# Kernel optimization log

Measured on AMD Instinct MI355X. Metric: run time of the kernel, lower is better.

Reference implementation:

```python
import jax, jax.numpy as jnp
import numpy as np

NEG_SLOPE = 0.2


def gat_conv(x, src, dst, W, a_src, a_dst, b, num_nodes):
    # x: [N, Fin], W: [Fin, Fout], a_src/a_dst: [Fout], b: [Fout]
    h = x @ W                                   # [N, Fout]
    alpha_s = h @ a_src                         # [N]
    alpha_d = h @ a_dst                         # [N]
    e = alpha_s[src] + alpha_d[dst]             # [E]
    e = jnp.where(e > 0, e, NEG_SLOPE * e)      # LeakyReLU(0.2)
    # segment softmax over edges grouped by destination node
    m = jax.ops.segment_max(e, dst, num_segments=num_nodes)   # [N]
    e = jnp.exp(e - m[dst])
    s = jax.ops.segment_sum(e, dst, num_segments=num_nodes)   # [N]
    alpha = e / s[dst]                          # [E] (every node has a self-loop)
    out = jax.ops.segment_sum(h[src] * alpha[:, None], dst, num_segments=num_nodes)
    return out + b


def setup_inputs() -> dict:
    key = jax.random.key(0)
    ks = jax.random.split(key, 10)
    N, E = 50000, 640000
    Fin, Fh, Fout = 128, 128, 64
    x = jax.random.normal(ks[0], (N, Fin), dtype=jnp.float32)
    edge_index = jax.random.randint(ks[1], (2, E), 0, N, dtype=jnp.int64)
    g = 1.0 / np.sqrt(Fin)
    W1 = jax.random.normal(ks[2], (Fin, Fh), dtype=jnp.float32) * g
    a1_src = jax.random.normal(ks[3], (Fh,), dtype=jnp.float32) * 0.1
    a1_dst = jax.random.normal(ks[4], (Fh,), dtype=jnp.float32) * 0.1
    b1 = jnp.zeros((Fh,), dtype=jnp.float32)
    g2 = 1.0 / np.sqrt(Fh)
    W2 = jax.random.normal(ks[5], (Fh, Fout), dtype=jnp.float32) * g2
    a2_src = jax.random.normal(ks[6], (Fout,), dtype=jnp.float32) * 0.1
    a2_dst = jax.random.normal(ks[7], (Fout,), dtype=jnp.float32) * 0.1
    b2 = jnp.zeros((Fout,), dtype=jnp.float32)
    return {"x": x, "edge_index": edge_index, "W1": W1, "a1_src": a1_src,
            "a1_dst": a1_dst, "b1": b1, "W2": W2, "a2_src": a2_src,
            "a2_dst": a2_dst, "b2": b2}


def reference(x, edge_index, W1, a1_src, a1_dst, b1, W2, a2_src, a2_dst, b2):
    N = x.shape[0]
    loops = jnp.arange(N, dtype=edge_index.dtype)
    src = jnp.concatenate([edge_index[0], loops])  # add self-loops (PyG default)
    dst = jnp.concatenate([edge_index[1], loops])
    h = gat_conv(x, src, dst, W1, a1_src, a1_dst, b1, N)
    h = jax.nn.relu(h)
    # F.dropout(0.1) skipped: deterministic (eval-mode) reference
    out = gat_conv(h, src, dst, W2, a2_src, a2_dst, b2, N)
    return out
```

## Files before the change

kernel.cpp:

```cpp
#include <hip/hip_runtime.h>

#define LEAK 0.2f

static __device__ __forceinline__ float leaky(float e) { return e > 0.f ? e : LEAK * e; }

static __device__ __forceinline__ unsigned f2bf(float f) {
    union { float f; unsigned u; } v; v.f = f;
    return (v.u + 0x7FFFu + ((v.u >> 16) & 1u)) >> 16;
}
static __device__ __forceinline__ float bflo(unsigned u) {
    union { unsigned x; float f; } v; v.x = u << 16; return v.f;
}
static __device__ __forceinline__ float bfhi(unsigned u) {
    union { unsigned x; float f; } v; v.x = u & 0xFFFF0000u; return v.f;
}

using bf16x8 = __attribute__((ext_vector_type(8))) short;
using f32x4 = __attribute__((ext_vector_type(4))) float;

__global__ __launch_bounds__(256) void k_prep(int* __restrict__ counts, int n,
                                              const int* __restrict__ ei, int nwords_check,
                                              int* __restrict__ flag,
                                              const float* __restrict__ W1,
                                              unsigned short* __restrict__ Wt1,
                                              const float* __restrict__ W2,
                                              unsigned short* __restrict__ Wt2, int NB) {
    int bid = blockIdx.x;
    int t = threadIdx.x;
    if (bid == 0) {
        if (t < 64) {
            int bad = 0;
            for (int i = 1 + 2 * t; i < nwords_check; i += 128) bad |= (ei[i] != 0);
            unsigned long long anybad = __ballot(bad != 0);
            if (t == 0) *flag = (anybad == 0ULL) ? 1 : 0;
        }
        return;
    }
    if (bid <= NB) {
        int i = (bid - 1) * 256 + t;
        if (i < n) counts[i] = 0;
        return;
    }
    if (bid <= NB + 4) {
        int q = bid - (NB + 1);
        int c = t & 127, ksub = t >> 7;
        int k0 = q * 32 + ksub * 16;
        union { unsigned short s[16]; uint4 v[2]; } u;
#pragma unroll
        for (int j = 0; j < 16; ++j) u.s[j] = (unsigned short)f2bf(W1[(size_t)(k0 + j) * 128 + c]);
        uint4* dst = (uint4*)(Wt1 + (size_t)c * 128 + k0);
        dst[0] = u.v[0];
        dst[1] = u.v[1];
        return;
    }
    {
        int q = bid - (NB + 5);
        int c = t & 63, ksub = t >> 6;
        int k0 = q * 64 + ksub * 16;
        union { unsigned short s[16]; uint4 v[2]; } u;
#pragma unroll
        for (int j = 0; j < 16; ++j) u.s[j] = (unsigned short)f2bf(W2[(size_t)(k0 + j) * 64 + c]);
        uint4* dst = (uint4*)(Wt2 + (size_t)c * 128 + k0);
        dst[0] = u.v[0];
        dst[1] = u.v[1];
        return;
    }
}

__global__ void k_count(const int* __restrict__ ei, const int* __restrict__ flag,
                        int* __restrict__ counts, int E) {
    int e = blockIdx.x * 256 + threadIdx.x;
    if (e >= E) return;
    int is64 = *flag;
    int d = is64 ? ei[(size_t)2 * E + 2 * e] : ei[(size_t)E + e];
    atomicAdd(&counts[d], 1);
}

__global__ void k_scan1(const int* __restrict__ counts, int* __restrict__ incl,
                        int* __restrict__ bsums, int n) {
    __shared__ int s[256];
    int t = threadIdx.x;
    int g = blockIdx.x * 256 + t;
    int v = (g < n) ? counts[g] : 0;
    s[t] = v;
    __syncthreads();
    for (int off = 1; off < 256; off <<= 1) {
        int add = (t >= off) ? s[t - off] : 0;
        __syncthreads();
        s[t] += add;
        __syncthreads();
    }
    if (g < n) incl[g] = s[t];
    if (t == 255) bsums[blockIdx.x] = s[255];
}

__global__ void k_scan2(int* __restrict__ bsums, int nb) {
    __shared__ int s[256];
    int t = threadIdx.x;
    int v = (t < nb) ? bsums[t] : 0;
    s[t] = v;
    __syncthreads();
    for (int off = 1; off < 256; off <<= 1) {
        int add = (t >= off) ? s[t - off] : 0;
        __syncthreads();
        s[t] += add;
        __syncthreads();
    }
    int excl = (t == 0) ? 0 : s[t - 1];
    if (t < nb) bsums[t] = excl;
}

__global__ void k_scan3(const int* __restrict__ incl, const int* __restrict__ bsums,
                        const int* __restrict__ counts, int* __restrict__ rowptr,
                        int* __restrict__ fillpos, int n) {
    int g = blockIdx.x * 256 + threadIdx.x;
    if (g < n) {
        int inc = incl[g] + bsums[blockIdx.x];
        rowptr[g + 1] = inc;
        fillpos[g] = inc - counts[g];
    }
    if (g == 0) rowptr[0] = 0;
}

__global__ void k_fill(const int* __restrict__ ei, const int* __restrict__ flag,
                       int* __restrict__ fillpos, int* __restrict__ colv, int E) {
    int e = blockIdx.x * 256 + threadIdx.x;
    if (e >= E) return;
    int is64 = *flag;
    int s = is64 ? ei[2 * e] : ei[e];
    int d = is64 ? ei[(size_t)2 * E + 2 * e] : ei[(size_t)E + e];
    int p = atomicAdd(&fillpos[d], 1);
    colv[p] = s;
}

template <int F, bool AF32>
__global__ __launch_bounds__(256) void k_gemm_mfma(const void* __restrict__ Xv,
                                                   const unsigned short* __restrict__ Wt,
                                                   const float* __restrict__ asrc,
                                                   const float* __restrict__ adst,
                                                   unsigned short* __restrict__ Hb,
                                                   float* __restrict__ out_s,
                                                   float* __restrict__ out_d, int n) {
    constexpr int K = 128;
    constexpr int KP = K + 8;
    constexpr int NT = F / 16;
    __shared__ unsigned short wsT[F * KP];
    int t = threadIdx.x;
    int w = t >> 6, lane = t & 63;
    int lrow = lane & 15, kg = lane >> 4;
    long long row0 = (long long)blockIdx.x * 64;

#pragma unroll
    for (int i = t; i < F * (K / 8); i += 256) {
        int c = i / (K / 8), j8 = i % (K / 8);
        uint4 v = ((const uint4*)(Wt + (size_t)c * K))[j8];
        *(uint4*)&wsT[c * KP + 8 * j8] = v;
    }
    __syncthreads();

    long long grow = row0 + w * 16 + lrow;
    bool rowok = grow < n;

    f32x4 acc[NT];
#pragma unroll
    for (int i = 0; i < NT; ++i) acc[i] = (f32x4){0.f, 0.f, 0.f, 0.f};

#pragma unroll
    for (int ks = 0; ks < K / 32; ++ks) {
        bf16x8 af;
        if constexpr (AF32) {
            const float* Xp = (const float*)Xv + grow * K + ks * 32 + kg * 8;
            float4 x0 = make_float4(0.f, 0.f, 0.f, 0.f), x1 = x0;
            if (rowok) {
                x0 = ((const float4*)Xp)[0];
                x1 = ((const float4*)Xp)[1];
            }
            af = (bf16x8){(short)f2bf(x0.x), (short)f2bf(x0.y), (short)f2bf(x0.z), (short)f2bf(x0.w),
                          (short)f2bf(x1.x), (short)f2bf(x1.y), (short)f2bf(x1.z), (short)f2bf(x1.w)};
        } else {
            uint4 u = make_uint4(0, 0, 0, 0);
            if (rowok) {
                const unsigned short* Xp = (const unsigned short*)Xv + grow * K + ks * 32 + kg * 8;
                u = *(const uint4*)Xp;
            }
            af = *(bf16x8*)&u;
        }
#pragma unroll
        for (int nt = 0; nt < NT; ++nt) {
            const unsigned short* bp = &wsT[(nt * 16 + lrow) * KP + ks * 32 + kg * 8];
            uint4 ub = *(const uint4*)bp;
            bf16x8 bf = *(bf16x8*)&ub;
            acc[nt] = __builtin_amdgcn_mfma_f32_16x16x32_bf16(af, bf, acc[nt], 0, 0, 0);
        }
    }

    {
        float ps[4] = {0.f, 0.f, 0.f, 0.f}, pd[4] = {0.f, 0.f, 0.f, 0.f};
#pragma unroll
        for (int nt = 0; nt < NT; ++nt) {
            float asv = asrc[nt * 16 + lrow];
            float adv = adst[nt * 16 + lrow];
#pragma unroll
            for (int i = 0; i < 4; ++i) {
                ps[i] = fmaf(acc[nt][i], asv, ps[i]);
                pd[i] = fmaf(acc[nt][i], adv, pd[i]);
            }
        }
#pragma unroll
        for (int off = 1; off < 16; off <<= 1) {
#pragma unroll
            for (int i = 0; i < 4; ++i) {
                ps[i] += __shfl_xor(ps[i], off);
                pd[i] += __shfl_xor(pd[i], off);
            }
        }
        if (lrow == 0) {
#pragma unroll
            for (int i = 0; i < 4; ++i) {
                long long r = row0 + w * 16 + kg * 4 + i;
                if (r < n) {
                    out_s[r] = ps[i];
                    out_d[r] = pd[i];
                }
            }
        }
    }

    int r0 = w * 16 + kg * 4;
#pragma unroll
    for (int nt = 0; nt < NT; ++nt) {
        int c = nt * 16 + lrow;
#pragma unroll
        for (int i = 0; i < 4; ++i) {
            long long r = row0 + r0 + i;
            if (r < n) Hb[r * F + c] = (unsigned short)f2bf(acc[nt][i]);
        }
    }
}

template <int F, bool RELU, bool OB>
__global__ __launch_bounds__(256) void k_agg(const int* __restrict__ rowptr,
                                             const int* __restrict__ colv,
                                             const float* __restrict__ as_,
                                             const float* __restrict__ ad_,
                                             const unsigned* __restrict__ Hu,
                                             const float* __restrict__ bias,
                                             void* __restrict__ OUT, int n) {
    constexpr int FG8 = F / 8;
    constexpr int GRP = 64 / FG8;
    int node = blockIdx.x * 4 + (threadIdx.x >> 6);
    int lane = threadIdx.x & 63;
    if (node >= n) return;
    int rs = rowptr[node], re = rowptr[node + 1];
    int deg = re - rs;
    float adi = ad_[node];
    float e_self = leaky(as_[node] + adi);

    int scol = node;
    float e_l = -3.0e38f;
    if (lane < deg) {
        scol = colv[rs + lane];
        e_l = leaky(as_[scol] + adi);
    }
    float m = fmaxf(e_l, e_self);
    for (int base = 64; base < deg; base += 64) {
        if (base + lane < deg) m = fmaxf(m, leaky(as_[colv[rs + base + lane]] + adi));
    }
#pragma unroll
    for (int off = 32; off; off >>= 1) m = fmaxf(m, __shfl_xor(m, off));

    float p_l = (lane < deg) ? __expf(e_l - m) : 0.f;
    float ssum = p_l;
    for (int base = 64; base < deg; base += 64) {
        if (base + lane < deg) ssum += __expf(leaky(as_[colv[rs + base + lane]] + adi) - m);
    }
#pragma unroll
    for (int off = 32; off; off >>= 1) ssum += __shfl_xor(ssum, off);
    float pself = __expf(e_self - m);
    ssum += pself;
    float inv = 1.f / ssum;
    float w_l = p_l * inv;
    float wself = pself * inv;

    int grp = lane / FG8;
    int fg = lane % FG8;
    const uint4* __restrict__ H16 = (const uint4*)Hu;
    float a0, a1, a2, a3, a4, a5, a6, a7;
    {
        uint4 hv = H16[(size_t)node * FG8 + fg];
        float ws0 = (grp == 0) ? wself : 0.f;
        a0 = ws0 * bflo(hv.x); a1 = ws0 * bfhi(hv.x);
        a2 = ws0 * bflo(hv.y); a3 = ws0 * bfhi(hv.y);
        a4 = ws0 * bflo(hv.z); a5 = ws0 * bfhi(hv.z);
        a6 = ws0 * bflo(hv.w); a7 = ws0 * bfhi(hv.w);
    }

    int cnt = deg < 64 ? deg : 64;
    constexpr int STEP = 4 * GRP;
    int cntr = (cnt + STEP - 1) / STEP * STEP;
#pragma unroll 1
    for (int i = 0; i < cntr; i += STEP) {
        int i0 = i + grp, i1 = i + GRP + grp, i2 = i + 2 * GRP + grp, i3 = i + 3 * GRP + grp;
        int s0 = __shfl(scol, i0), s1 = __shfl(scol, i1);
        int s2 = __shfl(scol, i2), s3 = __shfl(scol, i3);
        float w0 = __shfl(w_l, i0), w1 = __shfl(w_l, i1);
        float w2 = __shfl(w_l, i2), w3 = __shfl(w_l, i3);
        uint4 g0 = H16[(size_t)s0 * FG8 + fg];
        uint4 g1 = H16[(size_t)s1 * FG8 + fg];
        uint4 g2 = H16[(size_t)s2 * FG8 + fg];
        uint4 g3 = H16[(size_t)s3 * FG8 + fg];
        a0 = fmaf(w0, bflo(g0.x), a0); a1 = fmaf(w0, bfhi(g0.x), a1);
        a2 = fmaf(w0, bflo(g0.y), a2); a3 = fmaf(w0, bfhi(g0.y), a3);
        a4 = fmaf(w0, bflo(g0.z), a4); a5 = fmaf(w0, bfhi(g0.z), a5);
        a6 = fmaf(w0, bflo(g0.w), a6); a7 = fmaf(w0, bfhi(g0.w), a7);
        a0 = fmaf(w1, bflo(g1.x), a0); a1 = fmaf(w1, bfhi(g1.x), a1);
        a2 = fmaf(w1, bflo(g1.y), a2); a3 = fmaf(w1, bfhi(g1.y), a3);
        a4 = fmaf(w1, bflo(g1.z), a4); a5 = fmaf(w1, bfhi(g1.z), a5);
        a6 = fmaf(w1, bflo(g1.w), a6); a7 = fmaf(w1, bfhi(g1.w), a7);
        a0 = fmaf(w2, bflo(g2.x), a0); a1 = fmaf(w2, bfhi(g2.x), a1);
        a2 = fmaf(w2, bflo(g2.y), a2); a3 = fmaf(w2, bfhi(g2.y), a3);
        a4 = fmaf(w2, bflo(g2.z), a4); a5 = fmaf(w2, bfhi(g2.z), a5);
        a6 = fmaf(w2, bflo(g2.w), a6); a7 = fmaf(w2, bfhi(g2.w), a7);
        a0 = fmaf(w3, bflo(g3.x), a0); a1 = fmaf(w3, bfhi(g3.x), a1);
        a2 = fmaf(w3, bflo(g3.y), a2); a3 = fmaf(w3, bfhi(g3.y), a3);
        a4 = fmaf(w3, bflo(g3.z), a4); a5 = fmaf(w3, bfhi(g3.z), a5);
        a6 = fmaf(w3, bflo(g3.w), a6); a7 = fmaf(w3, bfhi(g3.w), a7);
    }
    for (int j = rs + 64; j < re; ++j) {
        int s = colv[j];
        float w = __expf(leaky(as_[s] + adi) - m) * inv;
        float we = (grp == 0) ? w : 0.f;
        uint4 g = H16[(size_t)s * FG8 + fg];
        a0 = fmaf(we, bflo(g.x), a0); a1 = fmaf(we, bfhi(g.x), a1);
        a2 = fmaf(we, bflo(g.y), a2); a3 = fmaf(we, bfhi(g.y), a3);
        a4 = fmaf(we, bflo(g.z), a4); a5 = fmaf(we, bfhi(g.z), a5);
        a6 = fmaf(we, bflo(g.w), a6); a7 = fmaf(we, bfhi(g.w), a7);
    }
#pragma unroll
    for (int off = FG8; off < 64; off <<= 1) {
        a0 += __shfl_xor(a0, off); a1 += __shfl_xor(a1, off);
        a2 += __shfl_xor(a2, off); a3 += __shfl_xor(a3, off);
        a4 += __shfl_xor(a4, off); a5 += __shfl_xor(a5, off);
        a6 += __shfl_xor(a6, off); a7 += __shfl_xor(a7, off);
    }
    if (grp == 0) {
        const float4* b4 = (const float4*)bias;
        float4 bv0 = b4[fg * 2], bv1 = b4[fg * 2 + 1];
        a0 += bv0.x; a1 += bv0.y; a2 += bv0.z; a3 += bv0.w;
        a4 += bv1.x; a5 += bv1.y; a6 += bv1.z; a7 += bv1.w;
        if (RELU) {
            a0 = fmaxf(a0, 0.f); a1 = fmaxf(a1, 0.f);
            a2 = fmaxf(a2, 0.f); a3 = fmaxf(a3, 0.f);
            a4 = fmaxf(a4, 0.f); a5 = fmaxf(a5, 0.f);
            a6 = fmaxf(a6, 0.f); a7 = fmaxf(a7, 0.f);
        }
        if (OB) {
            uint4 p;
            p.x = f2bf(a0) | (f2bf(a1) << 16);
            p.y = f2bf(a2) | (f2bf(a3) << 16);
            p.z = f2bf(a4) | (f2bf(a5) << 16);
            p.w = f2bf(a6) | (f2bf(a7) << 16);
            ((uint4*)OUT)[(size_t)node * FG8 + fg] = p;
        } else {
            float4* o4 = (float4*)((float*)OUT + (size_t)node * F + fg * 8);
            o4[0] = make_float4(a0, a1, a2, a3);
            o4[1] = make_float4(a4, a5, a6, a7);
        }
    }
}

extern "C" void kernel_launch(void* const* d_in, const int* in_sizes, int n_in,
                              void* d_out, int out_size, void* d_ws, size_t ws_size,
                              hipStream_t stream) {
    const float* x   = (const float*)d_in[0];
    const int*   ei  = (const int*)d_in[1];
    const float* W1  = (const float*)d_in[2];
    const float* a1s = (const float*)d_in[3];
    const float* a1d = (const float*)d_in[4];
    const float* b1  = (const float*)d_in[5];
    const float* W2  = (const float*)d_in[6];
    const float* a2s = (const float*)d_in[7];
    const float* a2d = (const float*)d_in[8];
    const float* b2  = (const float*)d_in[9];
    float* out = (float*)d_out;

    int N = in_sizes[0] / 128;
    int E = in_sizes[1] / 2;

    size_t off = 0;
    auto alloc = [&](size_t bytes) -> void* {
        off = (off + 255) & ~(size_t)255;
        void* p = (char*)d_ws + off;
        off += bytes;
        return p;
    };
    unsigned short* h = (unsigned short*)alloc((size_t)N * 128 * 2);
    unsigned short* out1b = (unsigned short*)alloc((size_t)N * 128 * 2);
    unsigned short* Wt1 = (unsigned short*)alloc(128 * 128 * 2);
    unsigned short* Wt2 = (unsigned short*)alloc(64 * 128 * 2);
    float* as_    = (float*)alloc((size_t)N * 4);
    float* ad_    = (float*)alloc((size_t)N * 4);
    int* counts   = (int*)alloc((size_t)N * 4);
    int* rowptr   = (int*)alloc((size_t)(N + 1) * 4);
    int* fillpos  = (int*)alloc((size_t)N * 4);
    int* incl     = (int*)alloc((size_t)N * 4);
    int* bsums    = (int*)alloc(1024);
    int* colv     = (int*)alloc((size_t)E * 4);
    int* flag     = (int*)alloc(256);

    int blocksE = (E + 255) / 256;
    int NB = (N + 255) / 256;
    int blocksN4 = (N + 3) / 4;
    int rowTiles = (N + 63) / 64;

    int nchk = 2 * E < 512 ? 2 * E : 512;
    k_prep<<<NB + 7, 256, 0, stream>>>(counts, N, ei, nchk, flag, W1, Wt1, W2, Wt2, NB);
    k_count<<<blocksE, 256, 0, stream>>>(ei, flag, counts, E);
    k_scan1<<<NB, 256, 0, stream>>>(counts, incl, bsums, N);
    k_scan2<<<1, 256, 0, stream>>>(bsums, NB);
    k_scan3<<<NB, 256, 0, stream>>>(incl, bsums, counts, rowptr, fillpos, N);
    k_fill<<<blocksE, 256, 0, stream>>>(ei, flag, fillpos, colv, E);

    k_gemm_mfma<128, true><<<rowTiles, 256, 0, stream>>>(x, Wt1, a1s, a1d, h, as_, ad_, N);
    k_agg<128, true, true><<<blocksN4, 256, 0, stream>>>(rowptr, colv, as_, ad_,
                                                         (const unsigned*)h, b1, out1b, N);

    k_gemm_mfma<64, false><<<rowTiles, 256, 0, stream>>>(out1b, Wt2, a2s, a2d, h, as_, ad_, N);
    k_agg<64, false, false><<<blocksN4, 256, 0, stream>>>(rowptr, colv, as_, ad_,
                                                          (const unsigned*)h, b2, out, N);
}
```

Measured before the change: 164.5 us.

## Build CSR with rank-from-count atomics instead of a second atomic fill pass

The count kernel now records each edge's atomic return value as its rank within its destination row, and stores compact int32 src/dst arrays. Placement then computes rowptr[dst]+rank without atomics, replacing the second pass of atomic increments on fillpos. Both edge kernels process four edges per thread with vectorized loads. The trade-off is three extra E-sized scratch arrays to write and read back, and the order of neighbours within a row now depends on atomic ordering.

```diff
diff --git a/kernel.cpp b/kernel.cpp
--- a/kernel.cpp
+++ b/kernel.cpp
@@ -67,13 +67,48 @@
     }
 }
 
-__global__ void k_count(const int* __restrict__ ei, const int* __restrict__ flag,
-                        int* __restrict__ counts, int E) {
-    int e = blockIdx.x * 256 + threadIdx.x;
-    if (e >= E) return;
+__global__ __launch_bounds__(256) void k_rank(const int* __restrict__ ei,
+                                              const int* __restrict__ flag,
+                                              int* __restrict__ counts,
+                                              int* __restrict__ rank_,
+                                              int* __restrict__ srcv,
+                                              int* __restrict__ dstv, int E) {
+    int base = (blockIdx.x * 256 + threadIdx.x) * 4;
+    if (base >= E) return;
     int is64 = *flag;
-    int d = is64 ? ei[(size_t)2 * E + 2 * e] : ei[(size_t)E + e];
-    atomicAdd(&counts[d], 1);
+    if (base + 3 < E) {
+        int s0, s1, s2, s3, d0, d1, d2, d3;
+        if (is64) {
+            const uint4* ps = (const uint4*)(ei + 2 * (size_t)base);
+            uint4 a = ps[0], b = ps[1];
+            const uint4* pd = (const uint4*)(ei + 2 * ((size_t)E + base));
+            uint4 c = pd[0], e4 = pd[1];
+            s0 = a.x; s1 = a.z; s2 = b.x; s3 = b.z;
+            d0 = c.x; d1 = c.z; d2 = e4.x; d3 = e4.z;
+        } else {
+            int4 a = *(const int4*)(ei + base);
+            int4 b = *(const int4*)(ei + (size_t)E + base);
+            s0 = a.x; s1 = a.y; s2 = a.z; s3 = a.w;
+            d0 = b.x; d1 = b.y; d2 = b.z; d3 = b.w;
+        }
+        int r0 = atomicAdd(&counts[d0], 1);
+        int r1 = atomicAdd(&counts[d1], 1);
+        int r2 = atomicAdd(&counts[d2], 1);
+        int r3 = atomicAdd(&counts[d3], 1);
+        *(int4*)(rank_ + base) = make_int4(r0, r1, r2, r3);
+        *(int4*)(srcv + base) = make_int4(s0, s1, s2, s3);
+        *(int4*)(dstv + base) = make_int4(d0, d1, d2, d3);
+    } else {
+        for (int j = 0; j < 4 && base + j < E; ++j) {
+            int e = base + j;
+            int ss = is64 ? ei[2 * (size_t)e] : ei[e];
+            int dd = is64 ? ei[2 * ((size_t)E + e)] : ei[(size_t)E + e];
+            int r = atomicAdd(&counts[dd], 1);
+            rank_[e] = r;
+            srcv[e] = ss;
+            dstv[e] = dd;
+        }
+    }
 }
 
 __global__ void k_scan1(const int* __restrict__ counts, int* __restrict__ incl,
@@ -111,26 +146,37 @@
 }
 
 __global__ void k_scan3(const int* __restrict__ incl, const int* __restrict__ bsums,
-                        const int* __restrict__ counts, int* __restrict__ rowptr,
-                        int* __restrict__ fillpos, int n) {
+                        int* __restrict__ rowptr, int n) {
     int g = blockIdx.x * 256 + threadIdx.x;
-    if (g < n) {
-        int inc = incl[g] + bsums[blockIdx.x];
-        rowptr[g + 1] = inc;
-        fillpos[g] = inc - counts[g];
-    }
+    if (g < n) rowptr[g + 1] = incl[g] + bsums[blockIdx.x];
     if (g == 0) rowptr[0] = 0;
 }
 
-__global__ void k_fill(const int* __restrict__ ei, const int* __restrict__ flag,
-                       int* __restrict__ fillpos, int* __restrict__ colv, int E) {
-    int e = blockIdx.x * 256 + threadIdx.x;
-    if (e >= E) return;
-    int is64 = *flag;
-    int s = is64 ? ei[2 * e] : ei[e];
-    int d = is64 ? ei[(size_t)2 * E + 2 * e] : ei[(size_t)E + e];
-    int p = atomicAdd(&fillpos[d], 1);
-    colv[p] = s;
+__global__ __launch_bounds__(256) void k_place(const int* __restrict__ rank_,
+                                               const int* __restrict__ srcv,
+                                               const int* __restrict__ dstv,
+                                               const int* __restrict__ rowptr,
+                                               int* __restrict__ colv, int E) {
+    int base = (blockIdx.x * 256 + threadIdx.x) * 4;
+    if (base >= E) return;
+    if (base + 3 < E) {
+        int4 r = *(const int4*)(rank_ + base);
+        int4 s = *(const int4*)(srcv + base);
+        int4 d = *(const int4*)(dstv + base);
+        int p0 = rowptr[d.x] + r.x;
+        int p1 = rowptr[d.y] + r.y;
+        int p2 = rowptr[d.z] + r.z;
+        int p3 = rowptr[d.w] + r.w;
+        colv[p0] = s.x;
+        colv[p1] = s.y;
+        colv[p2] = s.z;
+        colv[p3] = s.w;
+    } else {
+        for (int j = 0; j < 4 && base + j < E; ++j) {
+            int e = base + j;
+            colv[rowptr[dstv[e]] + rank_[e]] = srcv[e];
+        }
+    }
 }
 
 template <int F, bool AF32>
@@ -402,24 +448,26 @@
     float* ad_    = (float*)alloc((size_t)N * 4);
     int* counts   = (int*)alloc((size_t)N * 4);
     int* rowptr   = (int*)alloc((size_t)(N + 1) * 4);
-    int* fillpos  = (int*)alloc((size_t)N * 4);
     int* incl     = (int*)alloc((size_t)N * 4);
     int* bsums    = (int*)alloc(1024);
     int* colv     = (int*)alloc((size_t)E * 4);
+    int* rank_    = (int*)alloc((size_t)E * 4);
+    int* srcv     = (int*)alloc((size_t)E * 4);
+    int* dstv     = (int*)alloc((size_t)E * 4);
     int* flag     = (int*)alloc(256);
 
-    int blocksE = (E + 255) / 256;
     int NB = (N + 255) / 256;
     int blocksN4 = (N + 3) / 4;
     int rowTiles = (N + 63) / 64;
+    int blocksE4 = (E + 1023) / 1024;
 
     int nchk = 2 * E < 512 ? 2 * E : 512;
     k_prep<<<NB + 7, 256, 0, stream>>>(counts, N, ei, nchk, flag, W1, Wt1, W2, Wt2, NB);
-    k_count<<<blocksE, 256, 0, stream>>>(ei, flag, counts, E);
+    k_rank<<<blocksE4, 256, 0, stream>>>(ei, flag, counts, rank_, srcv, dstv, E);
     k_scan1<<<NB, 256, 0, stream>>>(counts, incl, bsums, N);
     k_scan2<<<1, 256, 0, stream>>>(bsums, NB);
-    k_scan3<<<NB, 256, 0, stream>>>(incl, bsums, counts, rowptr, fillpos, N);
-    k_fill<<<blocksE, 256, 0, stream>>>(ei, flag, fillpos, colv, E);
+    k_scan3<<<NB, 256, 0, stream>>>(incl, bsums, rowptr, N);
+    k_place<<<blocksE4, 256, 0, stream>>>(rank_, srcv, dstv, rowptr, colv, E);
 
     k_gemm_mfma<128, true><<<rowTiles, 256, 0, stream>>>(x, Wt1, a1s, a1d, h, as_, ad_, N);
     k_agg<128, true, true><<<blocksN4, 256, 0, stream>>>(rowptr, colv, as_, ad_,
```

New measurement: 139.7 us. -15.1%, faster.
